# Kernel tuning notes

Measured on AMD Instinct MI355X. Metric: run time of the kernel, lower is better.

The kernel has to match this reference:

```python
import jax, jax.numpy as jnp
import numpy as np

B, H, W, C = 2, 64, 64, 192
NUM_HEADS = 6
K = 7  # kernel_size, dilation = 1


def setup_inputs() -> dict:
    key = jax.random.key(0)
    ks = jax.random.split(key, 5)
    return {
        "x": jax.random.normal(ks[0], (B, H, W, C), dtype=jnp.float32),
        "w_qkv": jax.random.normal(ks[1], (3 * C, C), dtype=jnp.float32) * 0.02,
        "rpb": jax.random.normal(ks[2], (NUM_HEADS, 2 * K - 1, 2 * K - 1), dtype=jnp.float32) * 0.02,
        "temperature": jnp.ones((NUM_HEADS,), dtype=jnp.float32),
        "w_proj": jax.random.normal(ks[3], (C, C), dtype=jnp.float32) * 0.02,
    }


def reference(x, w_qkv, rpb, temperature, w_proj):
    b, h, w, c = x.shape
    hd = c // NUM_HEADS
    scale = hd ** (-0.5)

    # 1x1 conv qkv projection (pointwise linear over channels)
    qkv = jnp.einsum("bhwc,dc->bhwd", x, w_qkv)
    qkv = qkv.reshape(b, h, w, 3, NUM_HEADS, hd).transpose(3, 0, 4, 1, 2, 5)
    q, k, v = qkv[0], qkv[1], qkv[2]  # (B, nH, H, W, hd)
    q = q * scale

    # NATTEN neighborhood: window centered at each pixel, clamped to stay in-bounds
    si = jnp.clip(jnp.arange(h) - K // 2, 0, h - K)
    rows = si[:, None] + jnp.arange(K)          # (H, K) neighbor row indices
    sj = jnp.clip(jnp.arange(w) - K // 2, 0, w - K)
    cols = sj[:, None] + jnp.arange(K)          # (W, K) neighbor col indices

    # gather key/value neighborhoods: (B, nH, H, K, W, K, hd)
    k_nb = k[:, :, rows][:, :, :, :, cols]
    v_nb = v[:, :, rows][:, :, :, :, cols]

    # QK: (B, nH, H, W, Kh, Kw)
    attn = jnp.einsum("bnijd,bnikjld->bnijkl", q, k_nb)

    # relative position bias: index = neighbor - query + (K-1)
    ri = rows - jnp.arange(h)[:, None] + (K - 1)  # (H, K)
    rj = cols - jnp.arange(w)[:, None] + (K - 1)  # (W, K)
    bias = rpb[:, ri][:, :, :, rj]                # (nH, H, K, W, K)
    bias = bias.transpose(0, 1, 3, 2, 4)          # (nH, H, W, K, K)
    attn = attn + bias[None]

    attn = attn.reshape(b, NUM_HEADS, h, w, K * K)
    attn = attn * temperature[None, :, None, None, None]
    attn = jax.nn.softmax(attn, axis=-1)

    v_nb = v_nb.transpose(0, 1, 2, 4, 3, 5, 6).reshape(b, NUM_HEADS, h, w, K * K, hd)
    out = jnp.einsum("bnijp,bnijpd->bnijd", attn, v_nb)
    out = out.transpose(0, 2, 3, 1, 4).reshape(b, h, w, c)

    # 1x1 conv output projection
    return jnp.einsum("bhwc,dc->bhwd", out, w_proj)
```

## Files before the change

### kernel.cpp

```cpp
#include <hip/hip_runtime.h>
#include <hip/hip_bf16.h>
#include <math.h>

#define BB 2
#define HH 64
#define WW 64
#define CC 192
#define NH 6
#define HD 32
#define KS 7
#define NPIX (BB * HH * WW)
#define SCALE 0.17677669529663687f
#define GK 192

typedef __attribute__((ext_vector_type(8))) _Float16 f16x8;
typedef __attribute__((ext_vector_type(4))) _Float16 f16x4;
typedef __attribute__((ext_vector_type(2))) _Float16 h2;
typedef __attribute__((ext_vector_type(4))) float    f32x4;

#if defined(__has_builtin) && __has_builtin(__builtin_amdgcn_fdot2)
#define FDOT2(a, b, c) __builtin_amdgcn_fdot2((a), (b), (c), false)
#else
#define FDOT2(a, b, c) fmaf((float)(a)[0], (float)(b)[0], fmaf((float)(a)[1], (float)(b)[1], (c)))
#endif

#define LDH 104

__global__ __launch_bounds__(256) void gemm_mfma(const float* __restrict__ A,
                                                 const float* __restrict__ Bw,
                                                 float* __restrict__ Cm,
                                                 int M, int N) {
    __shared__ _Float16 As[64 * LDH];
    __shared__ _Float16 Bs[64 * LDH];

    const int t    = threadIdx.x;
    const int row0 = blockIdx.x * 64;
    const int col0 = blockIdx.y * 64;

    const int wave = t >> 6;
    const int wr   = wave >> 1;
    const int wc   = wave & 1;
    const int lane = t & 63;
    const int ln   = lane & 15;
    const int quad = lane >> 4;

    const int lr = t >> 2;
    const int ld = t & 3;

    f32x4 acc[2][2] = {};

#pragma unroll
    for (int kc = 0; kc < 2; ++kc) {
        if (kc) __syncthreads();
        const float* pa = A  + (size_t)(row0 + lr) * GK + kc * 96;
        const float* pb = Bw + (size_t)(col0 + lr) * GK + kc * 96;
#pragma unroll
        for (int u = 0; u < 6; ++u) {
            const int c4 = (u * 4 + ld) * 4;
            float4 a4 = *(const float4*)(pa + c4);
            float4 b4 = *(const float4*)(pb + c4);
            f16x4 ha = {(_Float16)a4.x, (_Float16)a4.y, (_Float16)a4.z, (_Float16)a4.w};
            f16x4 hb = {(_Float16)b4.x, (_Float16)b4.y, (_Float16)b4.z, (_Float16)b4.w};
            *(f16x4*)&As[lr * LDH + c4] = ha;
            *(f16x4*)&Bs[lr * LDH + c4] = hb;
        }
        __syncthreads();

#pragma unroll
        for (int ks = 0; ks < 3; ++ks) {
            const int k0 = ks * 32 + quad * 8;
            f16x8 af[2], bf[2];
#pragma unroll
            for (int mi = 0; mi < 2; ++mi)
                af[mi] = *(const f16x8*)&As[(wr * 32 + mi * 16 + ln) * LDH + k0];
#pragma unroll
            for (int ni = 0; ni < 2; ++ni)
                bf[ni] = *(const f16x8*)&Bs[(wc * 32 + ni * 16 + ln) * LDH + k0];
#pragma unroll
            for (int mi = 0; mi < 2; ++mi)
#pragma unroll
                for (int ni = 0; ni < 2; ++ni)
                    acc[mi][ni] = __builtin_amdgcn_mfma_f32_16x16x32_f16(
                        af[mi], bf[ni], acc[mi][ni], 0, 0, 0);
        }
    }

#pragma unroll
    for (int mi = 0; mi < 2; ++mi)
#pragma unroll
        for (int ni = 0; ni < 2; ++ni) {
            const int col = col0 + wc * 32 + ni * 16 + ln;
#pragma unroll
            for (int r = 0; r < 4; ++r) {
                const int row = row0 + wr * 32 + mi * 16 + quad * 4 + r;
                Cm[(size_t)row * N + col] = acc[mi][ni][r];
            }
        }
}

#define KSTR 20
#define VOFFU 1280
#define REGU 2560
#define PSTR 40

__global__ __launch_bounds__(256, 3) void natten_v3(const float* __restrict__ qkv,
                                                    const float* __restrict__ rpb,
                                                    const float* __restrict__ temperature,
                                                    float* __restrict__ out) {
    const int tid  = threadIdx.x;
    const int w    = tid >> 6;
    const int j    = tid & 63;
    const int i    = blockIdx.x & 63;
    const int head = (blockIdx.x >> 6) % NH;
    const int b    = blockIdx.x / (64 * NH);

    __shared__ unsigned region[4][REGU];
    __shared__ float srpb[169];
    if (tid < 169) srpb[tid] = rpb[head * 169 + tid];

    const float temp = temperature[head];
    const size_t pix = (size_t)b * 4096 + i * 64 + j;
    const float* qp = qkv + pix * 576 + head * HD;

    h2 qh[16];
#pragma unroll
    for (int d4 = 0; d4 < 8; ++d4) {
        float4 f = *(const float4*)(qp + d4 * 4);
        qh[d4 * 2 + 0] = h2{(_Float16)(f.x * SCALE), (_Float16)(f.y * SCALE)};
        qh[d4 * 2 + 1] = h2{(_Float16)(f.z * SCALE), (_Float16)(f.w * SCALE)};
    }

    __syncthreads();

    const int si = min(max(i - 3, 0), HH - KS);
    const int sj = min(max(j - 3, 0), WW - KS);

    float l = 0.f;
    float acc[HD];
#pragma unroll
    for (int d = 0; d < HD; ++d) acc[d] = 0.f;

    unsigned* kreg = region[w];
    unsigned* vreg = region[w] + VOFFU;

    const int nrows = (w < 3) ? 2 : 1;
    for (int t = 0; t < nrows; ++t) {
        const int ni = si + 2 * w + t;

        const float* rowk = qkv + ((size_t)b * 4096 + (size_t)ni * 64) * 576 + CC + head * HD;
#pragma unroll
        for (int it = 0; it < 4; ++it) {
            const int idx = j + (it << 6);
            const int px = idx >> 2, d = idx & 3;
            const float* src = rowk + px * 576 + d * 8;
            float4 k0 = *(const float4*)src;
            float4 k1 = *(const float4*)(src + 4);
            float4 v0 = *(const float4*)(src + CC);
            float4 v1 = *(const float4*)(src + CC + 4);
            f16x8 hk = {(_Float16)k0.x, (_Float16)k0.y, (_Float16)k0.z, (_Float16)k0.w,
                        (_Float16)k1.x, (_Float16)k1.y, (_Float16)k1.z, (_Float16)k1.w};
            f16x8 hv = {(_Float16)v0.x, (_Float16)v0.y, (_Float16)v0.z, (_Float16)v0.w,
                        (_Float16)v1.x, (_Float16)v1.y, (_Float16)v1.z, (_Float16)v1.w};
            *(f16x8*)&kreg[px * KSTR + d * 4] = hk;
            *(f16x8*)&vreg[px * KSTR + d * 4] = hv;
        }

        const float* rb = srpb + (ni - i + 6) * 13;
#pragma unroll
        for (int kj = 0; kj < 7; ++kj) {
            const int nj = sj + kj;

            float d0 = 0.f, d1 = 0.f, d2 = 0.f, d3 = 0.f;
#pragma unroll
            for (int c = 0; c < 4; ++c) {
                f16x8 kc = *(const f16x8*)&kreg[nj * KSTR + c * 4];
                const h2* kp = (const h2*)&kc;
                d0 = FDOT2(qh[c * 4 + 0], kp[0], d0);
                d1 = FDOT2(qh[c * 4 + 1], kp[1], d1);
                d2 = FDOT2(qh[c * 4 + 2], kp[2], d2);
                d3 = FDOT2(qh[c * 4 + 3], kp[3], d3);
            }
            const float dot = (d0 + d1) + (d2 + d3);
            const float logit = (dot + rb[nj - j + 6]) * temp;
            const float p = __expf(logit);
            l += p;

#pragma unroll
            for (int c = 0; c < 4; ++c) {
                f16x8 vc = *(const f16x8*)&vreg[nj * KSTR + c * 4];
#pragma unroll
                for (int e = 0; e < 8; ++e)
                    acc[c * 8 + e] = fmaf((float)vc[e], p, acc[c * 8 + e]);
            }
        }
    }

    if (w > 0) {
        float* pp = (float*)region[w] + j * PSTR;
#pragma unroll
        for (int d4 = 0; d4 < 8; ++d4)
            *(float4*)(pp + d4 * 4) = make_float4(acc[d4 * 4], acc[d4 * 4 + 1],
                                                  acc[d4 * 4 + 2], acc[d4 * 4 + 3]);
        pp[32] = l;
    }
    __syncthreads();
    if (w == 0) {
#pragma unroll
        for (int ww = 1; ww < 4; ++ww) {
            const float* pp = (const float*)region[ww] + j * PSTR;
#pragma unroll
            for (int d = 0; d < HD; ++d) acc[d] += pp[d];
            l += pp[32];
        }
        const float inv = 1.f / l;
        float* op = out + pix * CC + head * HD;
#pragma unroll
        for (int d4 = 0; d4 < 8; ++d4) {
            float4 o = make_float4(acc[d4 * 4 + 0] * inv, acc[d4 * 4 + 1] * inv,
                                   acc[d4 * 4 + 2] * inv, acc[d4 * 4 + 3] * inv);
            *(float4*)(op + d4 * 4) = o;
        }
    }
}

extern "C" void kernel_launch(void* const* d_in, const int* in_sizes, int n_in,
                              void* d_out, int out_size, void* d_ws, size_t ws_size,
                              hipStream_t stream) {
    const float* x           = (const float*)d_in[0];
    const float* w_qkv       = (const float*)d_in[1];
    const float* rpb         = (const float*)d_in[2];
    const float* temperature = (const float*)d_in[3];
    const float* w_proj      = (const float*)d_in[4];
    float* out = (float*)d_out;

    float* qkv      = (float*)d_ws;
    float* attn_out = qkv + (size_t)NPIX * 3 * CC;

    gemm_mfma<<<dim3(NPIX / 64, (3 * CC) / 64), 256, 0, stream>>>(
        x, w_qkv, qkv, NPIX, 3 * CC);

    natten_v3<<<dim3(BB * NH * HH), 256, 0, stream>>>(
        qkv, rpb, temperature, attn_out);

    gemm_mfma<<<dim3(NPIX / 64, CC / 64), 256, 0, stream>>>(
        attn_out, w_proj, out, NPIX, CC);
}
```

Baseline: 115.0 us.

## Store intermediates in fp16 and read MFMA operands directly from global memory

```diff
diff --git a/kernel.cpp b/kernel.cpp
--- a/kernel.cpp
+++ b/kernel.cpp
@@ -9,9 +9,8 @@
 #define NH 6
 #define HD 32
 #define KS 7
-#define NPIX (BB * HH * WW)
+#define NPIX 8192
 #define SCALE 0.17677669529663687f
-#define GK 192
 
 typedef __attribute__((ext_vector_type(8))) _Float16 f16x8;
 typedef __attribute__((ext_vector_type(4))) _Float16 f16x4;
@@ -24,65 +23,56 @@
 #define FDOT2(a, b, c) fmaf((float)(a)[0], (float)(b)[0], fmaf((float)(a)[1], (float)(b)[1], (c)))
 #endif
 
-#define LDH 104
-
-__global__ __launch_bounds__(256) void gemm_mfma(const float* __restrict__ A,
-                                                 const float* __restrict__ Bw,
-                                                 float* __restrict__ Cm,
-                                                 int M, int N) {
-    __shared__ _Float16 As[64 * LDH];
-    __shared__ _Float16 Bs[64 * LDH];
-
+#define XN   1572864
+#define OFF_XH  0
+#define OFF_WQ  1572864
+#define OFF_WP  1683456
+#define OFF_QKV 1720320
+#define OFF_ATT 6438912
+
+__global__ __launch_bounds__(256) void cvt_f16(const float* __restrict__ x,
+                                               const float* __restrict__ wq,
+                                               const float* __restrict__ wp,
+                                               _Float16* __restrict__ dst) {
+    const size_t off = ((size_t)blockIdx.x * 256 + threadIdx.x) * 4;
+    float4 v;
+    if (off < XN)                 v = *(const float4*)(x  + off);
+    else if (off < OFF_WP)        v = *(const float4*)(wq + (off - OFF_WQ));
+    else                          v = *(const float4*)(wp + (off - OFF_WP));
+    f16x4 h = {(_Float16)v.x, (_Float16)v.y, (_Float16)v.z, (_Float16)v.w};
+    *(f16x4*)(dst + off) = h;
+}
+
+__global__ __launch_bounds__(256) void gemm_h(const _Float16* __restrict__ A,
+                                              const _Float16* __restrict__ B,
+                                              _Float16* __restrict__ Ch,
+                                              float* __restrict__ Cf,
+                                              int N) {
     const int t    = threadIdx.x;
     const int row0 = blockIdx.x * 64;
     const int col0 = blockIdx.y * 64;
-
     const int wave = t >> 6;
     const int wr   = wave >> 1;
     const int wc   = wave & 1;
-    const int lane = t & 63;
-    const int ln   = lane & 15;
-    const int quad = lane >> 4;
-
-    const int lr = t >> 2;
-    const int ld = t & 3;
+    const int ln   = t & 15;
+    const int quad = (t & 63) >> 4;
 
     f32x4 acc[2][2] = {};
 
 #pragma unroll
-    for (int kc = 0; kc < 2; ++kc) {
-        if (kc) __syncthreads();
-        const float* pa = A  + (size_t)(row0 + lr) * GK + kc * 96;
-        const float* pb = Bw + (size_t)(col0 + lr) * GK + kc * 96;
-#pragma unroll
-        for (int u = 0; u < 6; ++u) {
-            const int c4 = (u * 4 + ld) * 4;
-            float4 a4 = *(const float4*)(pa + c4);
-            float4 b4 = *(const float4*)(pb + c4);
-            f16x4 ha = {(_Float16)a4.x, (_Float16)a4.y, (_Float16)a4.z, (_Float16)a4.w};
-            f16x4 hb = {(_Float16)b4.x, (_Float16)b4.y, (_Float16)b4.z, (_Float16)b4.w};
-            *(f16x4*)&As[lr * LDH + c4] = ha;
-            *(f16x4*)&Bs[lr * LDH + c4] = hb;
-        }
-        __syncthreads();
-
-#pragma unroll
-        for (int ks = 0; ks < 3; ++ks) {
-            const int k0 = ks * 32 + quad * 8;
-            f16x8 af[2], bf[2];
-#pragma unroll
-            for (int mi = 0; mi < 2; ++mi)
-                af[mi] = *(const f16x8*)&As[(wr * 32 + mi * 16 + ln) * LDH + k0];
+    for (int ks = 0; ks < 6; ++ks) {
+        const int k0 = ks * 32 + quad * 8;
+        f16x8 af[2], bf[2];
+        af[0] = *(const f16x8*)(A + (size_t)(row0 + wr * 32 + ln) * 192 + k0);
+        af[1] = *(const f16x8*)(A + (size_t)(row0 + wr * 32 + 16 + ln) * 192 + k0);
+        bf[0] = *(const f16x8*)(B + (size_t)(col0 + wc * 32 + ln) * 192 + k0);
+        bf[1] = *(const f16x8*)(B + (size_t)(col0 + wc * 32 + 16 + ln) * 192 + k0);
+#pragma unroll
+        for (int mi = 0; mi < 2; ++mi)
 #pragma unroll
             for (int ni = 0; ni < 2; ++ni)
-                bf[ni] = *(const f16x8*)&Bs[(wc * 32 + ni * 16 + ln) * LDH + k0];
-#pragma unroll
-            for (int mi = 0; mi < 2; ++mi)
-#pragma unroll
-                for (int ni = 0; ni < 2; ++ni)
-                    acc[mi][ni] = __builtin_amdgcn_mfma_f32_16x16x32_f16(
-                        af[mi], bf[ni], acc[mi][ni], 0, 0, 0);
-        }
+                acc[mi][ni] = __builtin_amdgcn_mfma_f32_16x16x32_f16(
+                    af[mi], bf[ni], acc[mi][ni], 0, 0, 0);
     }
 
 #pragma unroll
@@ -93,41 +83,43 @@
 #pragma unroll
             for (int r = 0; r < 4; ++r) {
                 const int row = row0 + wr * 32 + mi * 16 + quad * 4 + r;
-                Cm[(size_t)row * N + col] = acc[mi][ni][r];
+                if (Ch) Ch[(size_t)row * N + col] = (_Float16)acc[mi][ni][r];
+                else    Cf[(size_t)row * N + col] = acc[mi][ni][r];
             }
         }
 }
 
-#define KSTR 20
-#define VOFFU 1280
-#define REGU 2560
-#define PSTR 40
-
-__global__ __launch_bounds__(256, 3) void natten_v3(const float* __restrict__ qkv,
-                                                    const float* __restrict__ rpb,
-                                                    const float* __restrict__ temperature,
-                                                    float* __restrict__ out) {
+#define PL   264
+#define ROWU (8 * PL)
+
+__global__ __launch_bounds__(256) void natten_v4(const _Float16* __restrict__ qkv,
+                                                 const float* __restrict__ rpb,
+                                                 const float* __restrict__ temperature,
+                                                 _Float16* __restrict__ outh) {
     const int tid  = threadIdx.x;
     const int w    = tid >> 6;
     const int j    = tid & 63;
     const int i    = blockIdx.x & 63;
     const int head = (blockIdx.x >> 6) % NH;
-    const int b    = blockIdx.x / (64 * NH);
-
-    __shared__ unsigned region[4][REGU];
+    const int b    = blockIdx.x / 384;
+
+    __shared__ unsigned region[4][2][ROWU];
     __shared__ float srpb[169];
-    if (tid < 169) srpb[tid] = rpb[head * 169 + tid];
 
     const float temp = temperature[head];
-    const size_t pix = (size_t)b * 4096 + i * 64 + j;
-    const float* qp = qkv + pix * 576 + head * HD;
-
+    const float st   = SCALE * temp;
+    if (tid < 169) srpb[tid] = rpb[head * 169 + tid] * temp;
+
+    const int pix = b * 4096 + i * 64 + j;
+    const _Float16* qp = qkv + (size_t)pix * 576 + head * HD;
     h2 qh[16];
-#pragma unroll
-    for (int d4 = 0; d4 < 8; ++d4) {
-        float4 f = *(const float4*)(qp + d4 * 4);
-        qh[d4 * 2 + 0] = h2{(_Float16)(f.x * SCALE), (_Float16)(f.y * SCALE)};
-        qh[d4 * 2 + 1] = h2{(_Float16)(f.z * SCALE), (_Float16)(f.w * SCALE)};
+    {
+        uint4 q0 = *(const uint4*)(qp +  0);
+        uint4 q1 = *(const uint4*)(qp +  8);
+        uint4 q2 = *(const uint4*)(qp + 16);
+        uint4 q3 = *(const uint4*)(qp + 24);
+        *(uint4*)&qh[0]  = q0; *(uint4*)&qh[4]  = q1;
+        *(uint4*)&qh[8]  = q2; *(uint4*)&qh[12] = q3;
     }
 
     __syncthreads();
@@ -139,87 +131,87 @@
     float acc[HD];
 #pragma unroll
     for (int d = 0; d < HD; ++d) acc[d] = 0.f;
-
-    unsigned* kreg = region[w];
-    unsigned* vreg = region[w] + VOFFU;
 
     const int nrows = (w < 3) ? 2 : 1;
     for (int t = 0; t < nrows; ++t) {
         const int ni = si + 2 * w + t;
 
-        const float* rowk = qkv + ((size_t)b * 4096 + (size_t)ni * 64) * 576 + CC + head * HD;
-#pragma unroll
-        for (int it = 0; it < 4; ++it) {
+        const _Float16* rb0 = qkv + ((size_t)(b * 4096 + ni * 64)) * 576 + 192 + head * HD;
+        unsigned* reg = &region[w][t][0];
+#pragma unroll
+        for (int it = 0; it < 8; ++it) {
             const int idx = j + (it << 6);
-            const int px = idx >> 2, d = idx & 3;
-            const float* src = rowk + px * 576 + d * 8;
-            float4 k0 = *(const float4*)src;
-            float4 k1 = *(const float4*)(src + 4);
-            float4 v0 = *(const float4*)(src + CC);
-            float4 v1 = *(const float4*)(src + CC + 4);
-            f16x8 hk = {(_Float16)k0.x, (_Float16)k0.y, (_Float16)k0.z, (_Float16)k0.w,
-                        (_Float16)k1.x, (_Float16)k1.y, (_Float16)k1.z, (_Float16)k1.w};
-            f16x8 hv = {(_Float16)v0.x, (_Float16)v0.y, (_Float16)v0.z, (_Float16)v0.w,
-                        (_Float16)v1.x, (_Float16)v1.y, (_Float16)v1.z, (_Float16)v1.w};
-            *(f16x8*)&kreg[px * KSTR + d * 4] = hk;
-            *(f16x8*)&vreg[px * KSTR + d * 4] = hv;
-        }
-
-        const float* rb = srpb + (ni - i + 6) * 13;
+            const int px = idx >> 3, c = idx & 7;
+            uint4 d = *(const uint4*)(rb0 + (size_t)px * 576 + (c >> 2) * 192 + (c & 3) * 8);
+            *(uint4*)&reg[c * PL + px * 4] = d;
+        }
+
+        const float* rbias = srpb + (ni - i + 6) * 13;
 #pragma unroll
         for (int kj = 0; kj < 7; ++kj) {
             const int nj = sj + kj;
+            const unsigned* pp = reg + nj * 4;
+
+            h2 kh[16];
+            *(uint4*)&kh[0]  = *(const uint4*)(pp + 0 * PL);
+            *(uint4*)&kh[4]  = *(const uint4*)(pp + 1 * PL);
+            *(uint4*)&kh[8]  = *(const uint4*)(pp + 2 * PL);
+            *(uint4*)&kh[12] = *(const uint4*)(pp + 3 * PL);
 
             float d0 = 0.f, d1 = 0.f, d2 = 0.f, d3 = 0.f;
 #pragma unroll
             for (int c = 0; c < 4; ++c) {
-                f16x8 kc = *(const f16x8*)&kreg[nj * KSTR + c * 4];
-                const h2* kp = (const h2*)&kc;
-                d0 = FDOT2(qh[c * 4 + 0], kp[0], d0);
-                d1 = FDOT2(qh[c * 4 + 1], kp[1], d1);
-                d2 = FDOT2(qh[c * 4 + 2], kp[2], d2);
-                d3 = FDOT2(qh[c * 4 + 3], kp[3], d3);
+                d0 = FDOT2(qh[c * 4 + 0], kh[c * 4 + 0], d0);
+                d1 = FDOT2(qh[c * 4 + 1], kh[c * 4 + 1], d1);
+                d2 = FDOT2(qh[c * 4 + 2], kh[c * 4 + 2], d2);
+                d3 = FDOT2(qh[c * 4 + 3], kh[c * 4 + 3], d3);
             }
             const float dot = (d0 + d1) + (d2 + d3);
-            const float logit = (dot + rb[nj - j + 6]) * temp;
-            const float p = __expf(logit);
+            const float p = __expf(fmaf(dot, st, rbias[nj - j + 6]));
             l += p;
 
-#pragma unroll
-            for (int c = 0; c < 4; ++c) {
-                f16x8 vc = *(const f16x8*)&vreg[nj * KSTR + c * 4];
-#pragma unroll
-                for (int e = 0; e < 8; ++e)
-                    acc[c * 8 + e] = fmaf((float)vc[e], p, acc[c * 8 + e]);
+            h2 vh[16];
+            *(uint4*)&vh[0]  = *(const uint4*)(pp + 4 * PL);
+            *(uint4*)&vh[4]  = *(const uint4*)(pp + 5 * PL);
+            *(uint4*)&vh[8]  = *(const uint4*)(pp + 6 * PL);
+            *(uint4*)&vh[12] = *(const uint4*)(pp + 7 * PL);
+#pragma unroll
+            for (int c = 0; c < 16; ++c) {
+                acc[2 * c + 0] = fmaf((float)vh[c][0], p, acc[2 * c + 0]);
+                acc[2 * c + 1] = fmaf((float)vh[c][1], p, acc[2 * c + 1]);
             }
         }
     }
 
     if (w > 0) {
-        float* pp = (float*)region[w] + j * PSTR;
-#pragma unroll
-        for (int d4 = 0; d4 < 8; ++d4)
-            *(float4*)(pp + d4 * 4) = make_float4(acc[d4 * 4], acc[d4 * 4 + 1],
-                                                  acc[d4 * 4 + 2], acc[d4 * 4 + 3]);
-        pp[32] = l;
+        float* mp = (float*)&region[w][0][0] + j * 33;
+#pragma unroll
+        for (int d = 0; d < 32; ++d) mp[d] = acc[d];
+        mp[32] = l;
     }
     __syncthreads();
     if (w == 0) {
 #pragma unroll
         for (int ww = 1; ww < 4; ++ww) {
-            const float* pp = (const float*)region[ww] + j * PSTR;
-#pragma unroll
-            for (int d = 0; d < HD; ++d) acc[d] += pp[d];
-            l += pp[32];
+            const float* mp = (const float*)&region[ww][0][0] + j * 33;
+#pragma unroll
+            for (int d = 0; d < 32; ++d) acc[d] += mp[d];
+            l += mp[32];
         }
         const float inv = 1.f / l;
-        float* op = out + pix * CC + head * HD;
-#pragma unroll
-        for (int d4 = 0; d4 < 8; ++d4) {
-            float4 o = make_float4(acc[d4 * 4 + 0] * inv, acc[d4 * 4 + 1] * inv,
-                                   acc[d4 * 4 + 2] * inv, acc[d4 * 4 + 3] * inv);
-            *(float4*)(op + d4 * 4) = o;
-        }
+        _Float16* op = outh + (size_t)pix * CC + head * HD;
+        unsigned o[16];
+#pragma unroll
+        for (int c = 0; c < 16; ++c) {
+            h2 pk;
+            pk[0] = (_Float16)(acc[2 * c + 0] * inv);
+            pk[1] = (_Float16)(acc[2 * c + 1] * inv);
+            o[c] = *(unsigned*)&pk;
+        }
+        *(uint4*)(op +  0) = *(uint4*)&o[0];
+        *(uint4*)(op +  8) = *(uint4*)&o[4];
+        *(uint4*)(op + 16) = *(uint4*)&o[8];
+        *(uint4*)(op + 24) = *(uint4*)&o[12];
     }
 }
 
@@ -233,15 +225,18 @@
     const float* w_proj      = (const float*)d_in[4];
     float* out = (float*)d_out;
 
-    float* qkv      = (float*)d_ws;
-    float* attn_out = qkv + (size_t)NPIX * 3 * CC;
-
-    gemm_mfma<<<dim3(NPIX / 64, (3 * CC) / 64), 256, 0, stream>>>(
-        x, w_qkv, qkv, NPIX, 3 * CC);
-
-    natten_v3<<<dim3(BB * NH * HH), 256, 0, stream>>>(
-        qkv, rpb, temperature, attn_out);
-
-    gemm_mfma<<<dim3(NPIX / 64, CC / 64), 256, 0, stream>>>(
-        attn_out, w_proj, out, NPIX, CC);
-}
+    _Float16* hws    = (_Float16*)d_ws;
+    _Float16* x_h    = hws + OFF_XH;
+    _Float16* wq_h   = hws + OFF_WQ;
+    _Float16* wp_h   = hws + OFF_WP;
+    _Float16* qkv_h  = hws + OFF_QKV;
+    _Float16* attn_h = hws + OFF_ATT;
+
+    cvt_f16<<<dim3(1680), 256, 0, stream>>>(x, w_qkv, w_proj, hws);
+
+    gemm_h<<<dim3(128, 9), 256, 0, stream>>>(x_h, wq_h, qkv_h, nullptr, 3 * CC);
+
+    natten_v4<<<dim3(768), 256, 0, stream>>>(qkv_h, rpb, temperature, attn_h);
+
+    gemm_h<<<dim3(128, 3), 256, 0, stream>>>(attn_h, wp_h, nullptr, out, CC);
+}
```

New measurement: 114.4 us. About the same (-0.5%).
